# Performance work log

Hardware: AMD Instinct MI355X
Metric: run time of the kernel (lower is better)

Reference implementation:

```python
import jax, jax.numpy as jnp
import numpy as np

B, N, P, T = 64, 200, 400, 1200
TOPK, STRIDE = 3, 25
THRESHOLD = 0.3  # args.threshold
EPS = 1e-9


def setup_inputs() -> dict:
    key = jax.random.key(0)
    k1, k2, k3 = jax.random.split(key, 3)
    x = jax.random.normal(k1, (B, N, T), jnp.float32)
    # xavier_uniform with gain=1.414 on (P, N) parameter
    limit = 1.414 * np.sqrt(6.0 / (P + N))
    patterns = jax.random.uniform(k2, (P, N), jnp.float32, -limit, limit)
    length = jax.random.randint(k3, (B,), 500, T + 1).astype(jnp.int32)
    return {"x": x, "patterns": patterns, "length": length}


def _forward(x, patterns, length):
    # size after temporal max-pool, per sample
    size_after_pool = jnp.floor(length.astype(jnp.float32) / STRIDE)  # (B,)

    # L2-normalize the learned patterns (P, N)
    normalized_patterns = patterns / jnp.sqrt((patterns ** 2).sum(-1, keepdims=True) + EPS)

    # top_select: keep top-K entries by |value| along node dim
    _, topi = jax.lax.top_k(jnp.abs(normalized_patterns), TOPK)  # (P, K)
    mask = jnp.zeros((P, N), jnp.float32).at[jnp.arange(P)[:, None], topi].set(1.0)
    toppattern = mask * normalized_patterns  # (P, N)

    # HCP_static branch: frames = x.transpose(2,1) -> (B, T, N)
    frames = x.transpose(0, 2, 1)
    normalized_frames = frames / jnp.sqrt((frames ** 2).sum(-1, keepdims=True) + EPS)

    # cosine similarity of every frame to every pattern: (B, T, P)
    sim = jnp.einsum('btn,pn->btp', normalized_frames, normalized_patterns)

    # non-overlapping max-pool over time with kernel=stride=STRIDE
    simw = sim.transpose(0, 2, 1).reshape(B, P, T // STRIDE, STRIDE)  # (B,P,Tp,S)
    posscores = simw.max(-1)          # (B, P, Tp)
    negscores = (-simw).max(-1)       # (B, P, Tp)
    sap = size_after_pool[:, None, None]
    compos = (posscores / sap).sum(-1)  # (B, P)
    comneg = (negscores / sap).sum(-1)  # (B, P)
    PES = (compos + comneg) / 2.0       # (B, P)

    # graphs = key_patterns.T @ diag(PES) @ key_patterns * non_diag_scale
    key_patterns = jax.lax.stop_gradient(toppattern)  # detach
    c = TOPK * P / N
    non_diag_scale = jnp.full((N, N), c, jnp.float32) - jnp.eye(N, dtype=jnp.float32) * (c - 1.0)
    graphs = jnp.einsum('pn,bp,pm->bnm', key_patterns, PES, key_patterns) * non_diag_scale

    # SigLoss(normalized_patterns, toppattern)
    lenp = jnp.linalg.norm(normalized_patterns, axis=-1)
    lentopp = jnp.linalg.norm(toppattern, axis=-1)
    norm = ((1.0 - lentopp / lenp) ** 2).mean()

    # Relaxed_orthloss(normalized_patterns, threshold)
    simpp = (normalized_patterns @ normalized_patterns.T) * (1.0 - jnp.eye(P, dtype=jnp.float32))
    orth = (jax.nn.relu((jnp.abs(simpp) - THRESHOLD) / (1.0 - THRESHOLD + 1e-5)) ** 2).mean()

    return graphs, norm, orth


def reference(x, patterns, length):
    return _forward(x, patterns, length)
```

## Files before the change

kernel.cpp:

```cpp
#include <hip/hip_runtime.h>
#include <math.h>

#define B_ 64
#define N_ 200
#define P_ 400
#define T_ 1200
#define TPAD 1280
#define PPAD 512
#define STRIDE_ 25
#define EPS_ 1e-9f
#define KPAD 224
#define BSTRIDE 232

#define OFF_NPATT  0
#define OFF_NPB16  80000
#define OFF_KEYVAL 124800
#define OFF_KEYIDX 126400
#define OFF_PES    128000
#define OFF_NORMB  153600
#define OFF_ORTHB  153700
#define OFF_NORM   OFF_NORMB
#define OFF_ORTH   OFF_ORTHB
#define OFF_NPBT   153728
#define OFF_XN     211072
#define OFF_GPOOL  9386112
#define WS_FAST_FLOATS (9386112 + 2457600)

#define ZG_BLKS  40
#define ZP_BLKS  2
#define PAT_BLKS 100
#define TN_BLKS  (20 * B_)
#define Z_ALL    (ZG_BLKS + ZP_BLKS)
#define PREP_BLKS (Z_ALL + PAT_BLKS + TN_BLKS)

typedef float f4v __attribute__((ext_vector_type(4)));
typedef short s8v __attribute__((ext_vector_type(8)));

__device__ inline unsigned short f2bf(float f) {
    union { float f; unsigned u; } v; v.f = f;
    unsigned r = v.u + 0x7FFFu + ((v.u >> 16) & 1u);
    return (unsigned short)(r >> 16);
}
__device__ inline unsigned okey(float f) {
    unsigned u = __float_as_uint(f);
    return (u & 0x80000000u) ? ~u : (u | 0x80000000u);
}
__device__ inline float dekey(unsigned k) {
    unsigned u = (k & 0x80000000u) ? (k & 0x7fffffffu) : ~k;
    return __uint_as_float(u);
}

__device__ float pat_body(const float* __restrict__ patterns, float* __restrict__ ws,
                          int p, int lane) {
    float v0 = patterns[p * N_ + lane];
    float v1 = patterns[p * N_ + lane + 64];
    float v2 = patterns[p * N_ + lane + 128];
    float v3 = (lane < 8) ? patterns[p * N_ + lane + 192] : 0.0f;

    float ss = v0 * v0 + v1 * v1 + v2 * v2 + v3 * v3;
    for (int off = 32; off; off >>= 1) ss += __shfl_down(ss, off);
    ss = __shfl(ss, 0);

    float rn = 1.0f / sqrtf(ss + EPS_);
    float s0 = v0 * rn, s1 = v1 * rn, s2 = v2 * rn, s3 = v3 * rn;

    float* npatT = ws + OFF_NPATT;
    npatT[(lane) * P_ + p] = s0;
    npatT[(lane + 64) * P_ + p] = s1;
    npatT[(lane + 128) * P_ + p] = s2;
    if (lane < 8) npatT[(lane + 192) * P_ + p] = s3;

    unsigned short* npb = (unsigned short*)(ws + OFF_NPB16);
    unsigned short b0 = f2bf(s0), b1 = f2bf(s1), b2 = f2bf(s2), b3 = f2bf(s3);
    npb[p * KPAD + lane] = b0;
    npb[p * KPAD + lane + 64] = b1;
    npb[p * KPAD + lane + 128] = b2;
    if (lane < 8) npb[p * KPAD + lane + 192] = b3;
    if (lane < 24) npb[p * KPAD + 200 + lane] = 0;

    unsigned short* npbT = (unsigned short*)(ws + OFF_NPBT);
    {
        int k0 = lane, k1 = lane + 64, k2 = lane + 128;
        npbT[(k0 >> 3) * (PPAD * 8) + p * 8 + (k0 & 7)] = b0;
        npbT[(k1 >> 3) * (PPAD * 8) + p * 8 + (k1 & 7)] = b1;
        npbT[(k2 >> 3) * (PPAD * 8) + p * 8 + (k2 & 7)] = b2;
        if (lane < 8) {
            int k3 = lane + 192;
            npbT[(k3 >> 3) * (PPAD * 8) + p * 8 + (k3 & 7)] = b3;
        }
        if (lane < 24) {
            int k4 = 200 + lane;
            npbT[(k4 >> 3) * (PPAD * 8) + p * 8 + (k4 & 7)] = 0;
        }
    }

    float a0 = fabsf(s0), a1 = fabsf(s1), a2 = fabsf(s2), a3 = fabsf(s3);

    int ch0 = -1, ch1 = -1, ch2 = -1;
    float cs0 = 0.f, cs1 = 0.f, cs2 = 0.f;

    for (int r = 0; r < 3; r++) {
        float bv = -1.0f;
        int bi = 1 << 30;
        {
            int n = lane;
            bool sk = (n == ch0) || (n == ch1) || (n == ch2);
            if (!sk && a0 > bv) { bv = a0; bi = n; }
        }
        {
            int n = lane + 64;
            bool sk = (n == ch0) || (n == ch1) || (n == ch2);
            if (!sk && (a1 > bv || (a1 == bv && n < bi))) { bv = a1; bi = n; }
        }
        {
            int n = lane + 128;
            bool sk = (n == ch0) || (n == ch1) || (n == ch2);
            if (!sk && (a2 > bv || (a2 == bv && n < bi))) { bv = a2; bi = n; }
        }
        if (lane < 8) {
            int n = lane + 192;
            bool sk = (n == ch0) || (n == ch1) || (n == ch2);
            if (!sk && (a3 > bv || (a3 == bv && n < bi))) { bv = a3; bi = n; }
        }
        for (int off = 32; off; off >>= 1) {
            float ov = __shfl_down(bv, off);
            int oi = __shfl_down(bi, off);
            if (ov > bv || (ov == bv && oi < bi)) { bv = ov; bi = oi; }
        }
        bi = __shfl(bi, 0);
        int slot = bi >> 6, src = bi & 63;
        float mine = (slot == 0) ? s0 : (slot == 1) ? s1 : (slot == 2) ? s2 : s3;
        float sval = __shfl(mine, src);
        if (r == 0) { ch0 = bi; cs0 = sval; }
        else if (r == 1) { ch1 = bi; cs1 = sval; }
        else { ch2 = bi; cs2 = sval; }
    }

    float d2 = 0.f;
    if (lane == 0) {
        float* keyval = ws + OFF_KEYVAL;
        int* keyidx = (int*)(ws + OFF_KEYIDX);
        keyval[p * 4 + 0] = cs0; keyval[p * 4 + 1] = cs1; keyval[p * 4 + 2] = cs2;
        keyval[p * 4 + 3] = 0.f;
        keyidx[p * 4 + 0] = ch0; keyidx[p * 4 + 1] = ch1; keyidx[p * 4 + 2] = ch2;
        keyidx[p * 4 + 3] = -1;
        float lenp = sqrtf(ss) * rn;
        float lentopp = sqrtf(cs0 * cs0 + cs1 * cs1 + cs2 * cs2);
        float d = 1.0f - lentopp / lenp;
        d2 = d * d * (1.0f / (float)P_);
    }
    return d2;
}

__global__ __launch_bounds__(256) void prep_kernel(const float* __restrict__ x,
                                                   const float* __restrict__ patterns,
                                                   float* __restrict__ ws) {
    __shared__ unsigned short xt16[64 * 210];
    __shared__ float psums[256];
    __shared__ float rns[64];
    __shared__ float sh4[4];

    const int tid = threadIdx.x;

    if (blockIdx.x < Z_ALL) {
        int zb = blockIdx.x;
        if (zb < ZG_BLKS) {
            uint4* gp4 = (uint4*)(ws + OFF_GPOOL);
            int base = zb * 15360 + tid;
#pragma unroll
            for (int i = 0; i < 60; ++i)
                gp4[base + i * 256] = make_uint4(0, 0, 0, 0);
        } else {
            unsigned* p32 = (unsigned*)(ws + OFF_NPBT);
            int lb = zb - ZG_BLKS;
            for (int e = lb * 256 + tid; e < 12544; e += ZP_BLKS * 256) {
                int seg = e / 448, r32 = e % 448;
                p32[seg * 2048 + 1600 + r32] = 0u;
            }
        }
        return;
    }

    if (blockIdx.x < Z_ALL + PAT_BLKS) {
        int pblk = blockIdx.x - Z_ALL;
        int wv = tid >> 6, lane = tid & 63;
        int p = pblk * 4 + wv;
        float d2 = pat_body(patterns, ws, p, lane);
        if (lane == 0) sh4[wv] = d2;
        __syncthreads();
        if (tid == 0)
            ws[OFF_NORMB + pblk] = sh4[0] + sh4[1] + sh4[2] + sh4[3];
        return;
    }

    const int blk = blockIdx.x - Z_ALL - PAT_BLKS;
    const int t = tid & 63, r = tid >> 6;
    const int b = blk / 20;
    const int t0 = (blk % 20) * 64;
    const bool valid = (t0 + t) < T_;

    float ss = 0.0f;
    if (valid) {
        const float* xp = x + (size_t)b * N_ * T_ + t0 + t;
#pragma unroll 5
        for (int i = 0; i < 50; ++i) {
            int n = r * 50 + i;
            float v = xp[(size_t)n * T_];
            ss += v * v;
            xt16[t * 210 + n] = f2bf(v);
        }
    }
    psums[tid] = ss;
    __syncthreads();
    if (tid < 64) {
        float s = psums[tid] + psums[tid + 64] + psums[tid + 128] + psums[tid + 192];
        rns[tid] = rsqrtf(s + EPS_);
    }
    __syncthreads();

    unsigned short* xnT = (unsigned short*)(ws + OFF_XN);
#pragma unroll
    for (int j = 0; j < 7; ++j) {
        int idx = tid + 256 * j;
        int seg = idx >> 6, tt = idx & 63;
        s8v ov = (s8v){0, 0, 0, 0, 0, 0, 0, 0};
        if (seg < 25 && (t0 + tt) < T_) {
            float rn = rns[tt];
            const unsigned* src = (const unsigned*)&xt16[tt * 210 + seg * 8];
            unsigned o[4];
#pragma unroll
            for (int i = 0; i < 4; ++i) {
                unsigned u = src[i];
                float lo = __uint_as_float(u << 16) * rn;
                float hi = __uint_as_float(u & 0xffff0000u) * rn;
                o[i] = (unsigned)f2bf(lo) | ((unsigned)f2bf(hi) << 16);
            }
            ov = (s8v){(short)(o[0] & 0xffff), (short)(o[0] >> 16),
                       (short)(o[1] & 0xffff), (short)(o[1] >> 16),
                       (short)(o[2] & 0xffff), (short)(o[2] >> 16),
                       (short)(o[3] & 0xffff), (short)(o[3] >> 16)};
        }
        *(s8v*)(xnT + (((size_t)b * 28 + seg) * TPAD + t0 + tt) * 8) = ov;
    }
}

__global__ __launch_bounds__(256, 4) void work_kernel(float* __restrict__ ws,
                                                      unsigned* __restrict__ gpool) {
    __shared__ short ldsB[80 * BSTRIDE];
    __shared__ unsigned pool[2 * 7 * 80];

    const int tid = threadIdx.x;
    int orig = blockIdx.x;
    int xcd = orig & 7, rem = orig >> 3;
    int nid = (xcd < 4 ? xcd * 83 : 4 * 83 + (xcd - 4) * 82) + rem;

    const bool isOrth = (nid >= 640);
    int pb, mbg, b;
    if (isOrth) { int o = nid - 640; pb = o % 5; mbg = o / 5; b = 0; }
    else        { pb = nid % 5; mbg = (nid / 5) % 2; b = nid / 10; }

    const unsigned short* npb = (const unsigned short*)(ws + OFF_NPB16) + (size_t)(pb * 80) * KPAD;

#pragma unroll
    for (int j = 0; j < 9; ++j) {
        int idx = tid + 256 * j;
        if (idx < 2240) {
            int row = idx / 28, seg = idx % 28;
            *(s8v*)(&ldsB[row * BSTRIDE + seg * 8]) = *(const s8v*)(npb + (size_t)row * KPAD + seg * 8);
        }
    }
    for (int i = tid; i < 1120; i += 256) pool[i] = 0u;
    __syncthreads();

    const int wv = tid >> 6;
    const int lane = tid & 63;
    const int l15 = lane & 15, kg = lane >> 4;

    const int ROWS = isOrth ? PPAD : TPAD;
    const unsigned short* abase = isOrth
        ? (const unsigned short*)(ws + OFF_NPBT)
        : (const unsigned short*)(ws + OFF_XN) + (size_t)b * 28 * TPAD * 8;
    const int segstep = 4 * ROWS * 8;
    const int niter = isOrth ? 1 : 5;

    float orthpart = 0.f;

    for (int it = 0; it < niter; ++it) {
        const int mb = isOrth ? mbg : (mbg * 5 + it);
        const int row0 = mb * 128 + wv * 32 + l15;
        const unsigned short* ar0 = abase + ((size_t)kg * ROWS + row0) * 8;
        const unsigned short* ar1 = ar0 + 16 * 8;

        f4v acc[2][5];
#pragma unroll
        for (int mi = 0; mi < 2; ++mi)
#pragma unroll
            for (int ni = 0; ni < 5; ++ni) acc[mi][ni] = (f4v){0.f, 0.f, 0.f, 0.f};

        s8v A[4][2];
#pragma unroll
        for (int c = 0; c < 4; ++c) {
            A[c][0] = *(const s8v*)(ar0 + c * segstep);
            A[c][1] = *(const s8v*)(ar1 + c * segstep);
        }

#pragma unroll
        for (int c = 0; c < 7; ++c) {
            if (c + 4 < 7) {
                A[(c + 4) & 3][0] = *(const s8v*)(ar0 + (c + 4) * segstep);
                A[(c + 4) & 3][1] = *(const s8v*)(ar1 + (c + 4) * segstep);
            }
            s8v bf[5];
#pragma unroll
            for (int ni = 0; ni < 5; ++ni)
                bf[ni] = *(const s8v*)(&ldsB[(ni * 16 + l15) * BSTRIDE + c * 32 + kg * 8]);
#pragma unroll
            for (int ni = 0; ni < 5; ++ni) {
                acc[0][ni] = __builtin_amdgcn_mfma_f32_16x16x32_bf16(A[c & 3][0], bf[ni], acc[0][ni], 0, 0, 0);
                acc[1][ni] = __builtin_amdgcn_mfma_f32_16x16x32_bf16(A[c & 3][1], bf[ni], acc[1][ni], 0, 0, 0);
            }
        }

        if (isOrth) {
#pragma unroll
            for (int mi = 0; mi < 2; ++mi) {
                int rb = mb * 128 + wv * 32 + mi * 16 + kg * 4;
#pragma unroll
                for (int ni = 0; ni < 5; ++ni) {
                    int col = pb * 80 + ni * 16 + l15;
#pragma unroll
                    for (int jj = 0; jj < 4; ++jj) {
                        if (rb + jj == col) continue;
                        float t = (fabsf(acc[mi][ni][jj]) - 0.3f) * (1.0f / 0.70001f);
                        if (t > 0.0f) orthpart += t * t;
                    }
                }
            }
            break;
        }

        const int wbase = (mb * 128) / 25;
#pragma unroll
        for (int mi = 0; mi < 2; ++mi) {
            int f0 = mb * 128 + wv * 32 + mi * 16 + kg * 4;
            int w0 = f0 / 25, w3 = (f0 + 3) / 25;
            int wsplit = w3 * 25;
#pragma unroll
            for (int ni = 0; ni < 5; ++ni) {
                int pc = ni * 16 + l15;
                float p0 = -1e30f, p1 = -1e30f, n0 = -1e30f, n1 = -1e30f;
#pragma unroll
                for (int jj = 0; jj < 4; ++jj) {
                    float v = acc[mi][ni][jj];
                    if (f0 + jj < wsplit) { p0 = fmaxf(p0, v); n0 = fmaxf(n0, -v); }
                    else                 { p1 = fmaxf(p1, v); n1 = fmaxf(n1, -v); }
                }
                atomicMax(&pool[(0 * 7 + (w3 - wbase)) * 80 + pc], okey(p1));
                atomicMax(&pool[(1 * 7 + (w3 - wbase)) * 80 + pc], okey(n1));
                if (w0 != w3) {
                    atomicMax(&pool[(0 * 7 + (w0 - wbase)) * 80 + pc], okey(p0));
                    atomicMax(&pool[(1 * 7 + (w0 - wbase)) * 80 + pc], okey(n0));
                }
            }
        }
        __syncthreads();
        for (int e = tid; e < 1120; e += 256) {
            unsigned v = pool[e];
            pool[e] = 0u;
            if (!v) continue;
            int pass = e / 560, r2 = e % 560;
            int w = wbase + r2 / 80, p = r2 % 80;
            if (w < 48)
                atomicMax(&gpool[((size_t)(pass * B_ + b) * 48 + w) * 400 + pb * 80 + p], v);
        }
        __syncthreads();
    }

    if (isOrth) {
        for (int off = 32; off; off >>= 1) orthpart += __shfl_down(orthpart, off);
        __syncthreads();
        float* red = (float*)pool;
        if (lane == 0) red[wv] = orthpart;
        __syncthreads();
        if (tid == 0)
            ws[OFF_ORTHB + (nid - 640)] = (red[0] + red[1] + red[2] + red[3]) *
                                          (1.0f / ((float)P_ * (float)P_));
    }
}

__global__ __launch_bounds__(256) void pes_kernel(const unsigned* __restrict__ gpool,
                                                  const int* __restrict__ length,
                                                  float* __restrict__ ws) {
    int idx = blockIdx.x * 256 + threadIdx.x;
    if (idx >= B_ * P_) return;
    int b = idx / P_;
    int p = idx - b * P_;
    const unsigned* gp0 = gpool + (size_t)b * 48 * 400 + p;
    const unsigned* gp1 = gpool + (size_t)(B_ + b) * 48 * 400 + p;
    float s = 0.f;
#pragma unroll
    for (int w = 0; w < 48; ++w)
        s += dekey(gp0[w * 400]) + dekey(gp1[w * 400]);
    float rsap = 1.0f / (float)(length[b] / STRIDE_);
    ws[OFF_PES + b * P_ + p] = s * 0.5f * rsap;
}

__global__ __launch_bounds__(256) void graphs_row_kernel(const float* __restrict__ ws,
                                                         float* __restrict__ out) {
    __shared__ float rowbuf[8 * 200];
    __shared__ int   ki[400][4];
    __shared__ float kv[400][4];
    __shared__ float el[400];

    const int tid = threadIdx.x;
    const int b = blockIdx.x / 25;
    const int n0 = (blockIdx.x % 25) * 8;

    for (int i = tid; i < 1600; i += 256) rowbuf[i] = 0.f;
    for (int p = tid; p < 400; p += 256) {
        *(int4*)ki[p] = ((const int4*)(ws + OFF_KEYIDX))[p];
        *(float4*)kv[p] = ((const float4*)(ws + OFF_KEYVAL))[p];
        el[p] = ws[OFF_PES + b * P_ + p];
    }
    __syncthreads();

    for (int p = tid; p < 400; p += 256) {
        float e = el[p];
#pragma unroll
        for (int a = 0; a < 3; ++a) {
            int n = ki[p][a];
            if (n < n0 || n >= n0 + 8) continue;
            float va = kv[p][a] * e;
#pragma unroll
            for (int c = 0; c < 3; ++c) {
                float scale = (a == c) ? 1.0f : 6.0f;
                atomicAdd(&rowbuf[(n - n0) * 200 + ki[p][c]], va * kv[p][c] * scale);
            }
        }
    }
    __syncthreads();

    float4* dst = (float4*)(out + (size_t)b * N_ * N_ + (size_t)n0 * N_);
    const float4* srcb = (const float4*)rowbuf;
    for (int i = tid; i < 400; i += 256) dst[i] = srcb[i];

    if (blockIdx.x == 0 && tid == 0) {
        float sn = 0.f;
        for (int i = 0; i < PAT_BLKS; ++i) sn += ws[OFF_NORMB + i];
        float so = 0.f;
        for (int i = 0; i < 20; ++i) so += ws[OFF_ORTHB + i];
        out[(size_t)B_ * N_ * N_] = sn;
        out[(size_t)B_ * N_ * N_ + 1] = so;
    }
}

__global__ __launch_bounds__(256) void main_kernel(const float* __restrict__ x,
                                                   const int* __restrict__ length,
                                                   const float* __restrict__ ws,
                                                   float* __restrict__ pes) {
    __shared__ float xs[N_][STRIDE_ + 1];
    __shared__ float rnorm[STRIDE_];
    __shared__ float poolp[P_][5];
    __shared__ float pooln[P_][5];

    int w = blockIdx.x;
    int b = blockIdx.y;
    const float* xb = x + (size_t)b * N_ * T_ + (size_t)w * STRIDE_;

    for (int i = threadIdx.x; i < N_ * STRIDE_; i += 256) {
        int n = i / STRIDE_;
        int t = i - n * STRIDE_;
        xs[n][t] = xb[n * T_ + t];
    }
    __syncthreads();

    if (threadIdx.x < STRIDE_) {
        float ssf = 0.0f;
        for (int n = 0; n < N_; n++) { float vv = xs[n][threadIdx.x]; ssf += vv * vv; }
        rnorm[threadIdx.x] = 1.0f / sqrtf(ssf + EPS_);
    }
    __syncthreads();

    int pt = threadIdx.x % 50;
    int tt = threadIdx.x / 50;

    if (tt < 5) {
        float acc[8][5];
#pragma unroll
        for (int i = 0; i < 8; i++)
#pragma unroll
            for (int j = 0; j < 5; j++) acc[i][j] = 0.0f;

        const float4* np4 = (const float4*)(ws + OFF_NPATT);
        int pbq = pt * 2;
        for (int n = 0; n < N_; n++) {
            float4 q0 = np4[n * (P_ / 4) + pbq];
            float4 q1 = np4[n * (P_ / 4) + pbq + 1];
            float qa[8] = { q0.x, q0.y, q0.z, q0.w, q1.x, q1.y, q1.z, q1.w };
            float xv0 = xs[n][tt * 5 + 0];
            float xv1 = xs[n][tt * 5 + 1];
            float xv2 = xs[n][tt * 5 + 2];
            float xv3 = xs[n][tt * 5 + 3];
            float xv4 = xs[n][tt * 5 + 4];
#pragma unroll
            for (int i = 0; i < 8; i++) {
                acc[i][0] += qa[i] * xv0;
                acc[i][1] += qa[i] * xv1;
                acc[i][2] += qa[i] * xv2;
                acc[i][3] += qa[i] * xv3;
                acc[i][4] += qa[i] * xv4;
            }
        }
#pragma unroll
        for (int i = 0; i < 8; i++) {
            float pm = -1e30f, nm = -1e30f;
#pragma unroll
            for (int j = 0; j < 5; j++) {
                float s = acc[i][j] * rnorm[tt * 5 + j];
                pm = fmaxf(pm, s);
                nm = fmaxf(nm, -s);
            }
            poolp[pt * 8 + i][tt] = pm;
            pooln[pt * 8 + i][tt] = nm;
        }
    }
    __syncthreads();

    float rsap = 1.0f / (float)(length[b] / STRIDE_);
    for (int p = threadIdx.x; p < P_; p += 256) {
        float pm = poolp[p][0], nm = pooln[p][0];
#pragma unroll
        for (int q = 1; q < 5; q++) {
            pm = fmaxf(pm, poolp[p][q]);
            nm = fmaxf(nm, pooln[p][q]);
        }
        atomicAdd(&pes[b * P_ + p], (pm + nm) * 0.5f * rsap);
    }
}

__global__ __launch_bounds__(256) void fb_graphs_kernel(const float* __restrict__ ws,
                                                        float* __restrict__ out) {
    int idx = blockIdx.x * 256 + threadIdx.x;
    if (idx == 0) {
        out[(size_t)B_ * N_ * N_] = ws[OFF_NORM];
        out[(size_t)B_ * N_ * N_ + 1] = ws[OFF_ORTH];
    }
    if (idx >= B_ * P_) return;
    int b = idx / P_;
    int p = idx - b * P_;
    float e = ws[OFF_PES + b * P_ + p];
    const float* keyval = ws + OFF_KEYVAL;
    const int* keyidx = (const int*)(ws + OFF_KEYIDX);
    float va[3] = { keyval[p * 4 + 0], keyval[p * 4 + 1], keyval[p * 4 + 2] };
    int ia[3] = { keyidx[p * 4 + 0], keyidx[p * 4 + 1], keyidx[p * 4 + 2] };
    float* g = out + (size_t)b * N_ * N_;
#pragma unroll
    for (int a = 0; a < 3; a++)
#pragma unroll
        for (int c = 0; c < 3; c++) {
            float scale = (ia[a] == ia[c]) ? 1.0f : 6.0f;
            atomicAdd(&g[ia[a] * N_ + ia[c]], va[a] * va[c] * e * scale);
        }
}

__global__ __launch_bounds__(64) void pat_kernel(const float* __restrict__ patterns,
                                                 float* __restrict__ ws) {
    float d2 = pat_body(patterns, ws, blockIdx.x, threadIdx.x & 63);
    if (threadIdx.x == 0) atomicAdd(ws + OFF_NORM, d2);
}
__global__ __launch_bounds__(256) void orth_kernel(float* __restrict__ ws) {
    __shared__ float rowi[N_];
    __shared__ float red[256];
    const float* npatT = ws + OFF_NPATT;
    int i = blockIdx.x;
    for (int k = threadIdx.x; k < N_; k += 256) rowi[k] = npatT[k * P_ + i];
    __syncthreads();
    float partial = 0.0f;
    for (int j = threadIdx.x; j < P_; j += 256) {
        if (j == i) continue;
        float s = 0.0f;
        for (int k = 0; k < N_; k++) s += rowi[k] * npatT[k * P_ + j];
        float t = (fabsf(s) - 0.3f) * (1.0f / 0.70001f);
        if (t > 0.0f) partial += t * t;
    }
    red[threadIdx.x] = partial;
    __syncthreads();
    for (int sft = 128; sft; sft >>= 1) {
        if (threadIdx.x < sft) red[threadIdx.x] += red[threadIdx.x + sft];
        __syncthreads();
    }
    if (threadIdx.x == 0)
        atomicAdd(ws + OFF_ORTH, red[0] * (1.0f / ((float)P_ * (float)P_)));
}

extern "C" void kernel_launch(void* const* d_in, const int* in_sizes, int n_in,
                              void* d_out, int out_size, void* d_ws, size_t ws_size,
                              hipStream_t stream) {
    const float* x = (const float*)d_in[0];
    const float* patterns = (const float*)d_in[1];
    const int* length = (const int*)d_in[2];
    float* out = (float*)d_out;
    float* ws = (float*)d_ws;

    if (ws_size >= (size_t)WS_FAST_FLOATS * sizeof(float)) {
        unsigned* gpool = (unsigned*)(ws + OFF_GPOOL);
        prep_kernel<<<PREP_BLKS, 256, 0, stream>>>(x, patterns, ws);
        work_kernel<<<660, 256, 0, stream>>>(ws, gpool);
        pes_kernel<<<(B_ * P_ + 255) / 256, 256, 0, stream>>>(gpool, length, ws);
        graphs_row_kernel<<<B_ * 25, 256, 0, stream>>>(ws, out);
    } else {
        hipMemsetAsync(d_out, 0, (size_t)B_ * N_ * N_ * sizeof(float), stream);
        hipMemsetAsync(ws + OFF_PES, 0, (size_t)(B_ * P_) * sizeof(float), stream);
        hipMemsetAsync(ws + OFF_NORM, 0, sizeof(float), stream);
        hipMemsetAsync(ws + OFF_ORTH, 0, sizeof(float), stream);
        pat_kernel<<<P_, 64, 0, stream>>>(patterns, ws);
        orth_kernel<<<P_, 256, 0, stream>>>(ws);
        main_kernel<<<dim3(T_ / STRIDE_, B_), 256, 0, stream>>>(x, length, ws, ws + OFF_PES);
        fb_graphs_kernel<<<(B_ * P_ + 255) / 256, 256, 0, stream>>>(ws, out);
    }
}
```

Baseline: 68.18 us.

## Replace global atomic max-pool with per-tile partial stores merged in pes kernel

Work blocks now write their per-row-tile pooled max keys directly into a larger partial buffer indexed by row-block and window slot, instead of atomically maxing into a shared pooled array. This removes the need for the prep kernel to zero the global pool and drops the global atomics. The PES kernel then merges the overlapping tile partials for each window. Graph output stores also switch to nontemporal stores. The cost is a bigger workspace footprint and extra reads in the PES kernel.

```diff
diff --git a/kernel.cpp b/kernel.cpp
--- a/kernel.cpp
+++ b/kernel.cpp
@@ -24,16 +24,16 @@
 #define OFF_NPBT   153728
 #define OFF_XN     211072
 #define OFF_GPOOL  9386112
-#define WS_FAST_FLOATS (9386112 + 2457600)
-
-#define ZG_BLKS  40
+#define WS_FAST_FLOATS (9386112 + 3584000)
+
 #define ZP_BLKS  2
 #define PAT_BLKS 100
 #define TN_BLKS  (20 * B_)
-#define Z_ALL    (ZG_BLKS + ZP_BLKS)
+#define Z_ALL    ZP_BLKS
 #define PREP_BLKS (Z_ALL + PAT_BLKS + TN_BLKS)
 
 typedef float f4v __attribute__((ext_vector_type(4)));
+typedef unsigned u4v __attribute__((ext_vector_type(4)));
 typedef short s8v __attribute__((ext_vector_type(8)));
 
 __device__ inline unsigned short f2bf(float f) {
@@ -163,20 +163,11 @@
     const int tid = threadIdx.x;
 
     if (blockIdx.x < Z_ALL) {
-        int zb = blockIdx.x;
-        if (zb < ZG_BLKS) {
-            uint4* gp4 = (uint4*)(ws + OFF_GPOOL);
-            int base = zb * 15360 + tid;
-#pragma unroll
-            for (int i = 0; i < 60; ++i)
-                gp4[base + i * 256] = make_uint4(0, 0, 0, 0);
-        } else {
-            unsigned* p32 = (unsigned*)(ws + OFF_NPBT);
-            int lb = zb - ZG_BLKS;
-            for (int e = lb * 256 + tid; e < 12544; e += ZP_BLKS * 256) {
-                int seg = e / 448, r32 = e % 448;
-                p32[seg * 2048 + 1600 + r32] = 0u;
-            }
+        unsigned* p32 = (unsigned*)(ws + OFF_NPBT);
+        int lb = blockIdx.x;
+        for (int e = lb * 256 + tid; e < 12544; e += ZP_BLKS * 256) {
+            int seg = e / 448, r32 = e % 448;
+            p32[seg * 2048 + 1600 + r32] = 0u;
         }
         return;
     }
@@ -250,6 +241,7 @@
     __shared__ unsigned pool[2 * 7 * 80];
 
     const int tid = threadIdx.x;
+    const unsigned OKNEG = okey(-1e30f);
     int orig = blockIdx.x;
     int xcd = orig & 7, rem = orig >> 3;
     int nid = (xcd < 4 ? xcd * 83 : 4 * 83 + (xcd - 4) * 82) + rem;
@@ -269,7 +261,7 @@
             *(s8v*)(&ldsB[row * BSTRIDE + seg * 8]) = *(const s8v*)(npb + (size_t)row * KPAD + seg * 8);
         }
     }
-    for (int i = tid; i < 1120; i += 256) pool[i] = 0u;
+    for (int i = tid; i < 1120; i += 256) pool[i] = OKNEG;
     __syncthreads();
 
     const int wv = tid >> 6;
@@ -365,13 +357,10 @@
         }
         __syncthreads();
         for (int e = tid; e < 1120; e += 256) {
-            unsigned v = pool[e];
-            pool[e] = 0u;
-            if (!v) continue;
             int pass = e / 560, r2 = e % 560;
-            int w = wbase + r2 / 80, p = r2 % 80;
-            if (w < 48)
-                atomicMax(&gpool[((size_t)(pass * B_ + b) * 48 + w) * 400 + pb * 80 + p], v);
+            int slot = r2 / 80, pp = r2 % 80;
+            gpool[(((size_t)(pass * B_ + b)) * 10 + mb) * 2800 + slot * 400 + pb * 80 + pp] = pool[e];
+            pool[e] = OKNEG;
         }
         __syncthreads();
     }
@@ -395,12 +384,25 @@
     if (idx >= B_ * P_) return;
     int b = idx / P_;
     int p = idx - b * P_;
-    const unsigned* gp0 = gpool + (size_t)b * 48 * 400 + p;
-    const unsigned* gp1 = gpool + (size_t)(B_ + b) * 48 * 400 + p;
+
     float s = 0.f;
-#pragma unroll
-    for (int w = 0; w < 48; ++w)
-        s += dekey(gp0[w * 400]) + dekey(gp1[w * 400]);
+#pragma unroll 2
+    for (int pass = 0; pass < 2; ++pass) {
+        const unsigned* gp = gpool + ((size_t)(pass * B_ + b)) * 10 * 2800 + p;
+        for (int w = 0; w < 48; ++w) {
+            int a = 25 * w - 127;
+            int mb_lo = (a <= 0) ? 0 : ((a + 127) >> 7);
+            int mb_hi = (25 * w + 24) >> 7;
+            if (mb_hi > 9) mb_hi = 9;
+            unsigned k = 0u;
+            for (int mb = mb_lo; mb <= mb_hi; ++mb) {
+                int slot = w - (mb * 128) / 25;
+                unsigned v = gp[(size_t)mb * 2800 + slot * 400];
+                k = (v > k) ? v : k;
+            }
+            s += dekey(k);
+        }
+    }
     float rsap = 1.0f / (float)(length[b] / STRIDE_);
     ws[OFF_PES + b * P_ + p] = s * 0.5f * rsap;
 }
@@ -440,9 +442,10 @@
     }
     __syncthreads();
 
-    float4* dst = (float4*)(out + (size_t)b * N_ * N_ + (size_t)n0 * N_);
-    const float4* srcb = (const float4*)rowbuf;
-    for (int i = tid; i < 400; i += 256) dst[i] = srcb[i];
+    f4v* dst = (f4v*)(out + (size_t)b * N_ * N_ + (size_t)n0 * N_);
+    const f4v* srcb = (const f4v*)rowbuf;
+    for (int i = tid; i < 400; i += 256)
+        __builtin_nontemporal_store(srcb[i], dst + i);
 
     if (blockIdx.x == 0 && tid == 0) {
         float sn = 0.f;
@@ -609,10 +612,10 @@
         pes_kernel<<<(B_ * P_ + 255) / 256, 256, 0, stream>>>(gpool, length, ws);
         graphs_row_kernel<<<B_ * 25, 256, 0, stream>>>(ws, out);
     } else {
-        hipMemsetAsync(d_out, 0, (size_t)B_ * N_ * N_ * sizeof(float), stream);
-        hipMemsetAsync(ws + OFF_PES, 0, (size_t)(B_ * P_) * sizeof(float), stream);
-        hipMemsetAsync(ws + OFF_NORM, 0, sizeof(float), stream);
-        hipMemsetAsync(ws + OFF_ORTH, 0, sizeof(float), stream);
+        (void)hipMemsetAsync(d_out, 0, (size_t)B_ * N_ * N_ * sizeof(float), stream);
+        (void)hipMemsetAsync(ws + OFF_PES, 0, (size_t)(B_ * P_) * sizeof(float), stream);
+        (void)hipMemsetAsync(ws + OFF_NORM, 0, sizeof(float), stream);
+        (void)hipMemsetAsync(ws + OFF_ORTH, 0, sizeof(float), stream);
         pat_kernel<<<P_, 64, 0, stream>>>(patterns, ws);
         orth_kernel<<<P_, 256, 0, stream>>>(ws);
         main_kernel<<<dim3(T_ / STRIDE_, B_), 256, 0, stream>>>(x, length, ws, ws + OFF_PES);
```

After: 101.1 us. +48.3%, slower.
